# Kernel tuning notes

Measured on AMD Instinct MI355X. Metric: run time of the kernel, lower is better.

Reference implementation:

```python
import jax, jax.numpy as jnp
import numpy as np
from itertools import combinations

F = 24                 # num_fields
VOCAB_PER_FIELD = 10000
D = 16                 # embed_dim
B = 2048               # batch
FIELD_DIMS = [VOCAB_PER_FIELD] * F
TOTAL_VOCAB = sum(FIELD_DIMS)
# FeaturesEmbedding/FeaturesLinear offsets: cumulative field dims
OFFSETS = np.concatenate(([0], np.cumsum(FIELD_DIMS)[:-1])).astype(np.int64)  # (F,)
PAIRS = np.array(list(combinations(range(F), 2)), dtype=np.int64)   # (276, 2)
TRIPS = np.array(list(combinations(range(F), 3)), dtype=np.int64)   # (2024, 3)


def setup_inputs() -> dict:
    key = jax.random.key(0)
    k0, k1, k2, k3, k4 = jax.random.split(key, 5)
    x = jax.random.randint(k0, (B, F), 0, VOCAB_PER_FIELD)
    embed_table = jax.random.normal(k1, (TOTAL_VOCAB, D), dtype=jnp.float32) * 0.01
    lin_weight = jax.random.normal(k2, (TOTAL_VOCAB, 1), dtype=jnp.float32) * 0.01
    lin_bias = jnp.zeros((1,), dtype=jnp.float32)
    genotype_2nd = jax.random.normal(k3, (PAIRS.shape[0], 1), dtype=jnp.float32)
    genotype_3rd = jax.random.normal(k4, (TRIPS.shape[0], 1), dtype=jnp.float32)
    return {
        "x": x,
        "embed_table": embed_table,
        "lin_weight": lin_weight,
        "lin_bias": lin_bias,
        "genotype_2nd": genotype_2nd,
        "genotype_3rd": genotype_3rd,
    }


def reference(x, embed_table, lin_weight, lin_bias, genotype_2nd, genotype_3rd):
    idx = x + jnp.asarray(OFFSETS)[None, :]            # (B, F) global ids
    emb = embed_table[idx]                             # (B, F, D)
    # genotype is detached in the original forward
    g2 = jax.lax.stop_gradient(genotype_2nd)[:, 0]     # (P,)
    g3 = jax.lax.stop_gradient(genotype_3rd)[:, 0]     # (T,)
    # 2nd-order gated interactions: sum_t sum_d g2[t] * e_i * e_j
    p = emb[:, PAIRS[:, 0]]                            # (B, P, D)
    q = emb[:, PAIRS[:, 1]]
    nasfm_2nd = jnp.einsum('bpd,bpd,p->b', p, q, g2)   # (B,)
    # 3rd-order gated interactions
    p1 = emb[:, TRIPS[:, 0]]                           # (B, T, D)
    q1 = emb[:, TRIPS[:, 1]]
    r1 = emb[:, TRIPS[:, 2]]
    nasfm_3rd = jnp.einsum('btd,btd,btd,t->b', p1, q1, r1, g3)  # (B,)
    # FeaturesLinear: sum of per-feature weights + bias
    linear = jnp.sum(lin_weight[idx][..., 0], axis=1) + lin_bias[0]  # (B,)
    return jax.nn.sigmoid(linear + nasfm_2nd + nasfm_3rd)
```

## Files before the change

kernel.cpp:

```cpp
#include <hip/hip_runtime.h>
#include <math.h>

#define F 24
#define D 16
#define BATCH 2048
#define NPAIR 276
#define NTRIP 2024
#define VOCAB 10000
#define EPAD 17

__host__ __device__ constexpr int pair_base(int i) { return i * 23 - i * (i - 1) / 2; }
__host__ __device__ constexpr int pair_idx(int i, int j) { return pair_base(i) + (j - i - 1); }
__host__ __device__ constexpr int trip_base(int i) {
    return NTRIP - (24 - i) * (23 - i) * (22 - i) / 6;
}
__host__ __device__ constexpr int trip_idx(int i, int j, int k) {
    return trip_base(i) + (j - i - 1) * (46 - i - j) / 2 + (k - j - 1);
}
__host__ __device__ constexpr int pi_of(int p) {
    int i = 0;
    while (pair_base(i + 1) <= p) ++i;
    return i;
}

constexpr int CHUNK_B[17] = {0, 7, 23, 30, 46, 54, 70, 86, 95, 111, 127, 143, 160, 179, 201, 227, 276};

template <int C>
__device__ __forceinline__ float chunk_compute(const float* se,
                                               const float* __restrict__ g2,
                                               const float* __restrict__ g3) {
    constexpr int P0 = CHUNK_B[C], P1 = CHUNK_B[C + 1];
    constexpr int IMIN = pi_of(P0);
    constexpr int IMAX = pi_of(P1 - 1);
    float e[F];
#pragma unroll
    for (int f = IMIN; f < F; ++f) e[f] = se[f * EPAD];
    float acc = 0.f;
#pragma unroll
    for (int i = IMIN; i <= IMAX; ++i) {
#pragma unroll
        for (int j = i + 1; j < F; ++j) {
            if (pair_idx(i, j) >= P0 && pair_idx(i, j) < P1) {
                float pij = e[i] * e[j];
                acc = fmaf(g2[pair_idx(i, j)], pij, acc);
                float s = 0.f;
#pragma unroll
                for (int k = j + 1; k < F; ++k)
                    s = fmaf(g3[trip_idx(i, j, k)], e[k], s);
                acc = fmaf(pij, s, acc);
            }
        }
    }
    return acc;
}

__global__ __launch_bounds__(1024) void ctr_kernel(
    const int* __restrict__ x, const float* __restrict__ emb,
    const float* __restrict__ lw, const float* __restrict__ lb,
    const float* __restrict__ g2, const float* __restrict__ g3,
    float* __restrict__ out) {
    __shared__ float s_emb[4][F][EPAD];
    __shared__ float s_lw[4 * F];
    __shared__ float s_part[4][16];

    const int tid = threadIdx.x;
    const int row0 = blockIdx.x * 4;

    for (int t = tid; t < 4 * F * D; t += 1024) {
        int d = t & 15, seg = t >> 4;
        int f = seg % F, r = seg / F;
        int idx = x[(row0 + r) * F + f] + f * VOCAB;
        s_emb[r][f][d] = emb[idx * D + d];
    }
    for (int t = tid; t < 4 * F; t += 1024) {
        int f = t % F, r = t / F;
        s_lw[t] = lw[x[(row0 + r) * F + f] + f * VOCAB];
    }
    __syncthreads();

    const int d = tid & 15;
    const int r = (tid >> 4) & 3;
    const int w = tid >> 6;
    const float* se = &s_emb[r][0][d];

    float acc;
    switch (w) {
        case 0:  acc = chunk_compute<0>(se, g2, g3); break;
        case 1:  acc = chunk_compute<1>(se, g2, g3); break;
        case 2:  acc = chunk_compute<2>(se, g2, g3); break;
        case 3:  acc = chunk_compute<3>(se, g2, g3); break;
        case 4:  acc = chunk_compute<4>(se, g2, g3); break;
        case 5:  acc = chunk_compute<5>(se, g2, g3); break;
        case 6:  acc = chunk_compute<6>(se, g2, g3); break;
        case 7:  acc = chunk_compute<7>(se, g2, g3); break;
        case 8:  acc = chunk_compute<8>(se, g2, g3); break;
        case 9:  acc = chunk_compute<9>(se, g2, g3); break;
        case 10: acc = chunk_compute<10>(se, g2, g3); break;
        case 11: acc = chunk_compute<11>(se, g2, g3); break;
        case 12: acc = chunk_compute<12>(se, g2, g3); break;
        case 13: acc = chunk_compute<13>(se, g2, g3); break;
        case 14: acc = chunk_compute<14>(se, g2, g3); break;
        default: acc = chunk_compute<15>(se, g2, g3); break;
    }

#pragma unroll
    for (int m = 1; m < 16; m <<= 1) acc += __shfl_xor(acc, m, 64);
    if (d == 0) s_part[r][w] = acc;
    __syncthreads();

    if (tid < 64) {
        const int rr = tid >> 4, c = tid & 15;
        float v = s_part[rr][c];
#pragma unroll
        for (int m = 1; m < 16; m <<= 1) v += __shfl_xor(v, m, 64);
        if (c == 0) {
            float lin = lb[0];
#pragma unroll
            for (int f = 0; f < F; ++f) lin += s_lw[rr * F + f];
            float z = v + lin;
            out[row0 + rr] = 1.f / (1.f + __expf(-z));
        }
    }
}

extern "C" void kernel_launch(void* const* d_in, const int* in_sizes, int n_in,
                              void* d_out, int out_size, void* d_ws, size_t ws_size,
                              hipStream_t stream) {
    const int*   x   = (const int*)d_in[0];
    const float* emb = (const float*)d_in[1];
    const float* lw  = (const float*)d_in[2];
    const float* lb  = (const float*)d_in[3];
    const float* g2  = (const float*)d_in[4];
    const float* g3  = (const float*)d_in[5];
    float* out = (float*)d_out;

    hipLaunchKernelGGL(ctr_kernel, dim3(BATCH / 4), dim3(1024), 0, stream,
                       x, emb, lw, lb, g2, g3, out);
}
```

Measured before the change: 21.17 us.

## Repack gating weights into dense per-pair slots and loop uniformly

```diff
diff --git a/kernel.cpp b/kernel.cpp
--- a/kernel.cpp
+++ b/kernel.cpp
@@ -7,100 +7,104 @@
 #define NPAIR 276
 #define NTRIP 2024
 #define VOCAB 10000
-#define EPAD 17
+#define NSLOT 18
+#define SLOTF 28
+#define SLABF (F * D + 8)
 
 __host__ __device__ constexpr int pair_base(int i) { return i * 23 - i * (i - 1) / 2; }
-__host__ __device__ constexpr int pair_idx(int i, int j) { return pair_base(i) + (j - i - 1); }
 __host__ __device__ constexpr int trip_base(int i) {
     return NTRIP - (24 - i) * (23 - i) * (22 - i) / 6;
 }
 __host__ __device__ constexpr int trip_idx(int i, int j, int k) {
     return trip_base(i) + (j - i - 1) * (46 - i - j) / 2 + (k - j - 1);
 }
-__host__ __device__ constexpr int pi_of(int p) {
-    int i = 0;
-    while (pair_base(i + 1) <= p) ++i;
-    return i;
+__host__ __device__ constexpr int PB(int c) { return (NPAIR * c) / 16; }
+
+__global__ void repack_kernel(const float* __restrict__ g2,
+                              const float* __restrict__ g3,
+                              float* __restrict__ cw) {
+    int s = blockIdx.x * blockDim.x + threadIdx.x;
+    if (s >= 16 * NSLOT) return;
+    int c = s / NSLOT, q = s - c * NSLOT;
+    float* o = cw + s * SLOTF;
+    for (int t = 0; t < SLOTF; ++t) o[t] = 0.f;
+    int p = PB(c) + q;
+    if (p < PB(c + 1)) {
+        int i = 0;
+        while (pair_base(i + 1) <= p) ++i;
+        int j = i + 1 + (p - pair_base(i));
+        o[0] = __int_as_float(i);
+        o[1] = __int_as_float(j);
+        o[2] = g2[p];
+        if (j < 23) {
+            int tb = trip_idx(i, j, j + 1);
+            for (int k = j + 1; k < F; ++k) o[4 + k] = g3[tb + (k - j - 1)];
+        }
+    }
 }
 
-constexpr int CHUNK_B[17] = {0, 7, 23, 30, 46, 54, 70, 86, 95, 111, 127, 143, 160, 179, 201, 227, 276};
-
-template <int C>
-__device__ __forceinline__ float chunk_compute(const float* se,
-                                               const float* __restrict__ g2,
-                                               const float* __restrict__ g3) {
-    constexpr int P0 = CHUNK_B[C], P1 = CHUNK_B[C + 1];
-    constexpr int IMIN = pi_of(P0);
-    constexpr int IMAX = pi_of(P1 - 1);
-    float e[F];
-#pragma unroll
-    for (int f = IMIN; f < F; ++f) e[f] = se[f * EPAD];
-    float acc = 0.f;
-#pragma unroll
-    for (int i = IMIN; i <= IMAX; ++i) {
-#pragma unroll
-        for (int j = i + 1; j < F; ++j) {
-            if (pair_idx(i, j) >= P0 && pair_idx(i, j) < P1) {
-                float pij = e[i] * e[j];
-                acc = fmaf(g2[pair_idx(i, j)], pij, acc);
-                float s = 0.f;
-#pragma unroll
-                for (int k = j + 1; k < F; ++k)
-                    s = fmaf(g3[trip_idx(i, j, k)], e[k], s);
-                acc = fmaf(pij, s, acc);
-            }
-        }
-    }
-    return acc;
-}
-
-__global__ __launch_bounds__(1024) void ctr_kernel(
+__global__ __launch_bounds__(1024, 4) void ctr_main(
     const int* __restrict__ x, const float* __restrict__ emb,
     const float* __restrict__ lw, const float* __restrict__ lb,
-    const float* __restrict__ g2, const float* __restrict__ g3,
-    float* __restrict__ out) {
-    __shared__ float s_emb[4][F][EPAD];
+    const float* __restrict__ cw, float* __restrict__ out) {
+    __shared__ float s_e[4 * SLABF];
+    __shared__ int   s_idx[4 * F];
     __shared__ float s_lw[4 * F];
     __shared__ float s_part[4][16];
 
     const int tid = threadIdx.x;
     const int row0 = blockIdx.x * 4;
 
-    for (int t = tid; t < 4 * F * D; t += 1024) {
-        int d = t & 15, seg = t >> 4;
-        int f = seg % F, r = seg / F;
+    if (tid < 4 * F) {
+        int r = tid / F, f = tid - r * F;
         int idx = x[(row0 + r) * F + f] + f * VOCAB;
-        s_emb[r][f][d] = emb[idx * D + d];
+        s_idx[tid] = idx;
+        s_lw[tid] = lw[idx];
     }
-    for (int t = tid; t < 4 * F; t += 1024) {
-        int f = t % F, r = t / F;
-        s_lw[t] = lw[x[(row0 + r) * F + f] + f * VOCAB];
+    __syncthreads();
+
+    if (tid < 4 * F * 4) {
+        int seg = tid >> 2, q = tid & 3;
+        int r = seg / F, f = seg - r * F;
+        float4 v = reinterpret_cast<const float4*>(emb)[s_idx[seg] * 4 + q];
+        float* b = &s_e[r * SLABF + f * D + q * 4];
+        b[0] = v.x; b[1] = v.y; b[2] = v.z; b[3] = v.w;
     }
     __syncthreads();
 
     const int d = tid & 15;
     const int r = (tid >> 4) & 3;
-    const int w = tid >> 6;
-    const float* se = &s_emb[r][0][d];
+    const int w = __builtin_amdgcn_readfirstlane(tid >> 6);
+    const float* se = &s_e[r * SLABF];
 
-    float acc;
-    switch (w) {
-        case 0:  acc = chunk_compute<0>(se, g2, g3); break;
-        case 1:  acc = chunk_compute<1>(se, g2, g3); break;
-        case 2:  acc = chunk_compute<2>(se, g2, g3); break;
-        case 3:  acc = chunk_compute<3>(se, g2, g3); break;
-        case 4:  acc = chunk_compute<4>(se, g2, g3); break;
-        case 5:  acc = chunk_compute<5>(se, g2, g3); break;
-        case 6:  acc = chunk_compute<6>(se, g2, g3); break;
-        case 7:  acc = chunk_compute<7>(se, g2, g3); break;
-        case 8:  acc = chunk_compute<8>(se, g2, g3); break;
-        case 9:  acc = chunk_compute<9>(se, g2, g3); break;
-        case 10: acc = chunk_compute<10>(se, g2, g3); break;
-        case 11: acc = chunk_compute<11>(se, g2, g3); break;
-        case 12: acc = chunk_compute<12>(se, g2, g3); break;
-        case 13: acc = chunk_compute<13>(se, g2, g3); break;
-        case 14: acc = chunk_compute<14>(se, g2, g3); break;
-        default: acc = chunk_compute<15>(se, g2, g3); break;
+    float e[F];
+#pragma unroll
+    for (int f = 0; f < F; ++f) e[f] = se[f * D + d];
+
+    const float4* cp = reinterpret_cast<const float4*>(cw) + w * (NSLOT * 7);
+    float acc = 0.f;
+#pragma unroll 2
+    for (int s = 0; s < NSLOT; ++s) {
+        float4 h  = cp[s * 7 + 0];
+        float4 c0 = cp[s * 7 + 1], c1 = cp[s * 7 + 2], c2 = cp[s * 7 + 3];
+        float4 c3 = cp[s * 7 + 4], c4 = cp[s * 7 + 5], c5 = cp[s * 7 + 6];
+        int i = __float_as_int(h.x), j = __float_as_int(h.y);
+        float ei = se[i * D + d];
+        float ej = se[j * D + d];
+        float ta = h.z, tb = 0.f;
+        ta = fmaf(c0.x, e[0],  ta); tb = fmaf(c0.y, e[1],  tb);
+        ta = fmaf(c0.z, e[2],  ta); tb = fmaf(c0.w, e[3],  tb);
+        ta = fmaf(c1.x, e[4],  ta); tb = fmaf(c1.y, e[5],  tb);
+        ta = fmaf(c1.z, e[6],  ta); tb = fmaf(c1.w, e[7],  tb);
+        ta = fmaf(c2.x, e[8],  ta); tb = fmaf(c2.y, e[9],  tb);
+        ta = fmaf(c2.z, e[10], ta); tb = fmaf(c2.w, e[11], tb);
+        ta = fmaf(c3.x, e[12], ta); tb = fmaf(c3.y, e[13], tb);
+        ta = fmaf(c3.z, e[14], ta); tb = fmaf(c3.w, e[15], tb);
+        ta = fmaf(c4.x, e[16], ta); tb = fmaf(c4.y, e[17], tb);
+        ta = fmaf(c4.z, e[18], ta); tb = fmaf(c4.w, e[19], tb);
+        ta = fmaf(c5.x, e[20], ta); tb = fmaf(c5.y, e[21], tb);
+        ta = fmaf(c5.z, e[22], ta); tb = fmaf(c5.w, e[23], tb);
+        acc = fmaf(ei * ej, ta + tb, acc);
     }
 
 #pragma unroll
@@ -109,7 +113,7 @@
     __syncthreads();
 
     if (tid < 64) {
-        const int rr = tid >> 4, c = tid & 15;
+        int rr = tid >> 4, c = tid & 15;
         float v = s_part[rr][c];
 #pragma unroll
         for (int m = 1; m < 16; m <<= 1) v += __shfl_xor(v, m, 64);
@@ -133,7 +137,9 @@
     const float* g2  = (const float*)d_in[4];
     const float* g3  = (const float*)d_in[5];
     float* out = (float*)d_out;
+    float* cw  = (float*)d_ws;
 
-    hipLaunchKernelGGL(ctr_kernel, dim3(BATCH / 4), dim3(1024), 0, stream,
-                       x, emb, lw, lb, g2, g3, out);
+    hipLaunchKernelGGL(repack_kernel, dim3(2), dim3(256), 0, stream, g2, g3, cw);
+    hipLaunchKernelGGL(ctr_main, dim3(BATCH / 4), dim3(1024), 0, stream,
+                       x, emb, lw, lb, cw, out);
 }
```

Result: faster. 19.80 us (-6.5%).

## Transpose shared embedding layout, vectorize gathers and register loads

Applied to the files above, without the earlier changes.

```diff
diff --git a/kernel.cpp b/kernel.cpp
--- a/kernel.cpp
+++ b/kernel.cpp
@@ -7,7 +7,7 @@
 #define NPAIR 276
 #define NTRIP 2024
 #define VOCAB 10000
-#define EPAD 17
+#define EPAD 28
 
 __host__ __device__ constexpr int pair_base(int i) { return i * 23 - i * (i - 1) / 2; }
 __host__ __device__ constexpr int pair_idx(int i, int j) { return pair_base(i) + (j - i - 1); }
@@ -17,27 +17,17 @@
 __host__ __device__ constexpr int trip_idx(int i, int j, int k) {
     return trip_base(i) + (j - i - 1) * (46 - i - j) / 2 + (k - j - 1);
 }
-__host__ __device__ constexpr int pi_of(int p) {
-    int i = 0;
-    while (pair_base(i + 1) <= p) ++i;
-    return i;
-}
 
 constexpr int CHUNK_B[17] = {0, 7, 23, 30, 46, 54, 70, 86, 95, 111, 127, 143, 160, 179, 201, 227, 276};
 
 template <int C>
-__device__ __forceinline__ float chunk_compute(const float* se,
+__device__ __forceinline__ float chunk_compute(const float (&e)[F],
                                                const float* __restrict__ g2,
                                                const float* __restrict__ g3) {
     constexpr int P0 = CHUNK_B[C], P1 = CHUNK_B[C + 1];
-    constexpr int IMIN = pi_of(P0);
-    constexpr int IMAX = pi_of(P1 - 1);
-    float e[F];
-#pragma unroll
-    for (int f = IMIN; f < F; ++f) e[f] = se[f * EPAD];
     float acc = 0.f;
 #pragma unroll
-    for (int i = IMIN; i <= IMAX; ++i) {
+    for (int i = 0; i < 23; ++i) {
 #pragma unroll
         for (int j = i + 1; j < F; ++j) {
             if (pair_idx(i, j) >= P0 && pair_idx(i, j) < P1) {
@@ -54,63 +44,80 @@
     return acc;
 }
 
-__global__ __launch_bounds__(1024) void ctr_kernel(
+__global__ __launch_bounds__(1024, 4) void ctr_main(
     const int* __restrict__ x, const float* __restrict__ emb,
     const float* __restrict__ lw, const float* __restrict__ lb,
     const float* __restrict__ g2, const float* __restrict__ g3,
     float* __restrict__ out) {
-    __shared__ float s_emb[4][F][EPAD];
+    __shared__ float s_e[4 * D * EPAD];
+    __shared__ int   s_idx[4 * F];
     __shared__ float s_lw[4 * F];
-    __shared__ float s_part[4][16];
+    __shared__ float s_part[16][4];
 
     const int tid = threadIdx.x;
     const int row0 = blockIdx.x * 4;
 
-    for (int t = tid; t < 4 * F * D; t += 1024) {
-        int d = t & 15, seg = t >> 4;
-        int f = seg % F, r = seg / F;
+    if (tid < 4 * F) {
+        int r = tid / F, f = tid - r * F;
         int idx = x[(row0 + r) * F + f] + f * VOCAB;
-        s_emb[r][f][d] = emb[idx * D + d];
+        s_idx[tid] = idx;
+        s_lw[tid] = lw[idx];
     }
-    for (int t = tid; t < 4 * F; t += 1024) {
-        int f = t % F, r = t / F;
-        s_lw[t] = lw[x[(row0 + r) * F + f] + f * VOCAB];
+    __syncthreads();
+
+    if (tid < 4 * F * 4) {
+        int seg = tid >> 2, q = tid & 3;
+        int r = seg / F, f = seg - r * F;
+        float4 v = reinterpret_cast<const float4*>(emb)[s_idx[seg] * 4 + q];
+        s_e[(r * D + q * 4 + 0) * EPAD + f] = v.x;
+        s_e[(r * D + q * 4 + 1) * EPAD + f] = v.y;
+        s_e[(r * D + q * 4 + 2) * EPAD + f] = v.z;
+        s_e[(r * D + q * 4 + 3) * EPAD + f] = v.w;
     }
     __syncthreads();
 
     const int d = tid & 15;
     const int r = (tid >> 4) & 3;
     const int w = tid >> 6;
-    const float* se = &s_emb[r][0][d];
+
+    float e[F];
+    {
+        const float4* se4 = reinterpret_cast<const float4*>(&s_e[(r * D + d) * EPAD]);
+#pragma unroll
+        for (int n = 0; n < 6; ++n) {
+            float4 v = se4[n];
+            e[4 * n] = v.x; e[4 * n + 1] = v.y; e[4 * n + 2] = v.z; e[4 * n + 3] = v.w;
+        }
+    }
 
     float acc;
     switch (w) {
-        case 0:  acc = chunk_compute<0>(se, g2, g3); break;
-        case 1:  acc = chunk_compute<1>(se, g2, g3); break;
-        case 2:  acc = chunk_compute<2>(se, g2, g3); break;
-        case 3:  acc = chunk_compute<3>(se, g2, g3); break;
-        case 4:  acc = chunk_compute<4>(se, g2, g3); break;
-        case 5:  acc = chunk_compute<5>(se, g2, g3); break;
-        case 6:  acc = chunk_compute<6>(se, g2, g3); break;
-        case 7:  acc = chunk_compute<7>(se, g2, g3); break;
-        case 8:  acc = chunk_compute<8>(se, g2, g3); break;
-        case 9:  acc = chunk_compute<9>(se, g2, g3); break;
-        case 10: acc = chunk_compute<10>(se, g2, g3); break;
-        case 11: acc = chunk_compute<11>(se, g2, g3); break;
-        case 12: acc = chunk_compute<12>(se, g2, g3); break;
-        case 13: acc = chunk_compute<13>(se, g2, g3); break;
-        case 14: acc = chunk_compute<14>(se, g2, g3); break;
-        default: acc = chunk_compute<15>(se, g2, g3); break;
+        case 0:  acc = chunk_compute<0>(e, g2, g3); break;
+        case 1:  acc = chunk_compute<1>(e, g2, g3); break;
+        case 2:  acc = chunk_compute<2>(e, g2, g3); break;
+        case 3:  acc = chunk_compute<3>(e, g2, g3); break;
+        case 4:  acc = chunk_compute<4>(e, g2, g3); break;
+        case 5:  acc = chunk_compute<5>(e, g2, g3); break;
+        case 6:  acc = chunk_compute<6>(e, g2, g3); break;
+        case 7:  acc = chunk_compute<7>(e, g2, g3); break;
+        case 8:  acc = chunk_compute<8>(e, g2, g3); break;
+        case 9:  acc = chunk_compute<9>(e, g2, g3); break;
+        case 10: acc = chunk_compute<10>(e, g2, g3); break;
+        case 11: acc = chunk_compute<11>(e, g2, g3); break;
+        case 12: acc = chunk_compute<12>(e, g2, g3); break;
+        case 13: acc = chunk_compute<13>(e, g2, g3); break;
+        case 14: acc = chunk_compute<14>(e, g2, g3); break;
+        default: acc = chunk_compute<15>(e, g2, g3); break;
     }
 
 #pragma unroll
     for (int m = 1; m < 16; m <<= 1) acc += __shfl_xor(acc, m, 64);
-    if (d == 0) s_part[r][w] = acc;
+    if (d == 0) s_part[w][r] = acc;
     __syncthreads();
 
     if (tid < 64) {
         const int rr = tid >> 4, c = tid & 15;
-        float v = s_part[rr][c];
+        float v = s_part[c][rr];
 #pragma unroll
         for (int m = 1; m < 16; m <<= 1) v += __shfl_xor(v, m, 64);
         if (c == 0) {
@@ -134,6 +141,6 @@
     const float* g3  = (const float*)d_in[5];
     float* out = (float*)d_out;
 
-    hipLaunchKernelGGL(ctr_kernel, dim3(BATCH / 4), dim3(1024), 0, stream,
+    hipLaunchKernelGGL(ctr_main, dim3(BATCH / 4), dim3(1024), 0, stream,
                        x, emb, lw, lb, g2, g3, out);
 }
```

Result: slower. 21.86 us (+3.3%).
